# Kernel tuning notes

Measured on AMD Instinct MI355X. Metric: run time of the kernel, lower is better.

## Reference

```python
import jax, jax.numpy as jnp
import numpy as np

B, J, E = 4096, 32, 256

def setup_inputs() -> dict:
    key = jax.random.key(0)
    ks = jax.random.split(key, 7)
    return {
        "x": jax.random.normal(ks[0], (B, E), dtype=jnp.float32),
        "state": jax.random.normal(ks[1], (B, J * E), dtype=jnp.float32),
        "keys": jax.random.normal(ks[2], (J, E), dtype=jnp.float32) * 0.1,
        "U": jax.random.normal(ks[3], (E, E), dtype=jnp.float32) * 0.1,
        "V": jax.random.normal(ks[4], (E, E), dtype=jnp.float32) * 0.1,
        "W": jax.random.normal(ks[5], (E, E), dtype=jnp.float32) * 0.1,
        "bias": jax.random.normal(ks[6], (E,), dtype=jnp.float32) * 0.1,
    }

def reference(x, state, keys, U, V, W, bias):
    b, je = state.shape
    j = keys.shape[0]
    e = x.shape[1]
    s = state.reshape(b, j, e)                      # [B,J,E]
    # gate_j = sigmoid(<x, state_j> + <x, key_j>)
    gate = jax.nn.sigmoid(jnp.einsum('be,bje->bj', x, s)
                          + x @ keys.T)             # [B,J]
    # candidate_j = relu(U s_j + bias + W x + V k_j)
    cand = jax.nn.relu(jnp.einsum('bje,fe->bjf', s, U)
                       + bias
                       + (x @ W.T)[:, None, :]
                       + (keys @ V.T)[None, :, :])  # [B,J,E]
    s_next = s + gate[..., None] * cand
    norm = jnp.abs(jnp.linalg.norm(s_next, axis=-1, keepdims=True)) + 1e-8
    s_next = s_next / norm
    return s_next.reshape(b, je)
```

## Files before the change

kernel.cpp:

```cpp
#include <hip/hip_runtime.h>
#include <hip/hip_bf16.h>

typedef __bf16 bf16_t;
typedef __attribute__((ext_vector_type(8))) __bf16 bf16x8;
typedef __attribute__((ext_vector_type(4))) __bf16 bf16x4;
typedef __attribute__((ext_vector_type(4))) float f32x4;

#define E_DIM 256
#define J_DIM 32
#define B_DIM 4096
#define M_DIM (B_DIM * J_DIM)

#define XK_BLOCKS 512
#define CVT_BLOCKS 64
#define VKB_BLOCKS 32
#define PREP_GRID (XK_BLOCKS + 2 * CVT_BLOCKS + VKB_BLOCKS)

#define XK_LDA (E_DIM + 4)
#define LDB 40

__global__ __launch_bounds__(256) void prep_kernel(
    const float* __restrict__ x, const float* __restrict__ keys,
    const float* __restrict__ U, const float* __restrict__ V,
    const float* __restrict__ W, const float* __restrict__ bias,
    float* __restrict__ xk, float* __restrict__ vkb,
    bf16_t* __restrict__ Ubf, bf16_t* __restrict__ Wbf) {
    __shared__ float smem[(J_DIM + 8) * XK_LDA];
    int tid = threadIdx.x;
    int bid = blockIdx.x;
    if (bid < XK_BLOCKS) {
        float* sK = smem;
        float* sX = smem + J_DIM * XK_LDA;
        int b0 = bid * 8;
#pragma unroll
        for (int it = 0; it < 8; ++it) {
            int t = it * 256 + tid;
            int r = t >> 6, c = (t & 63) * 4;
            *(f32x4*)(sK + r * XK_LDA + c) = *(const f32x4*)(keys + (size_t)r * E_DIM + c);
        }
#pragma unroll
        for (int it = 0; it < 2; ++it) {
            int t = it * 256 + tid;
            int r = t >> 6, c = (t & 63) * 4;
            *(f32x4*)(sX + r * XK_LDA + c) =
                *(const f32x4*)(x + (size_t)(b0 + r) * E_DIM + c);
        }
        __syncthreads();
        int j = tid & 31, bl = tid >> 5;
        float acc = 0.f;
        for (int e = 0; e < E_DIM; e += 4) {
            f32x4 xv = *(const f32x4*)(sX + bl * XK_LDA + e);
            f32x4 kv = *(const f32x4*)(sK + j * XK_LDA + e);
#pragma unroll
            for (int i = 0; i < 4; ++i) acc += xv[i] * kv[i];
        }
        xk[(size_t)(b0 + bl) * J_DIM + j] = acc;
    } else if (bid < XK_BLOCKS + 2 * CVT_BLOCKS) {
        int cb = bid - XK_BLOCKS;
        const float* src = (cb < CVT_BLOCKS) ? U : W;
        bf16_t* dst = (cb < CVT_BLOCKS) ? Ubf : Wbf;
        int idx = (cb & (CVT_BLOCKS - 1)) * 1024 + tid * 4;
        f32x4 v = *(const f32x4*)(src + idx);
        bf16x4 o;
#pragma unroll
        for (int i = 0; i < 4; ++i) o[i] = (bf16_t)v[i];
        *(bf16x4*)(dst + idx) = o;
    } else {
        int j = bid - (XK_BLOCKS + 2 * CVT_BLOCKS);
        int f = tid;
        float* sk = smem;
        sk[f] = keys[(size_t)j * E_DIM + f];
        __syncthreads();
        float acc = bias[f];
        for (int e = 0; e < E_DIM; e += 4) {
            f32x4 vv = *(const f32x4*)(V + (size_t)f * E_DIM + e);
#pragma unroll
            for (int i = 0; i < 4; ++i) acc += vv[i] * sk[e + i];
        }
        vkb[(size_t)j * E_DIM + f] = acc;
    }
}

__global__ __launch_bounds__(256) void memcell_kernel(
    const float* __restrict__ x, const float* __restrict__ state,
    const bf16_t* __restrict__ Ubf, const bf16_t* __restrict__ Wbf,
    const float* __restrict__ xk, const float* __restrict__ vkb,
    float* __restrict__ out) {
    __shared__ __align__(16) bf16_t sB[2][E_DIM][LDB];
    int tid = threadIdx.x;
    int w = tid >> 6, lane = tid & 63, quad = lane >> 4, l15 = lane & 15;
    int m0 = blockIdx.x * 64;
    int bw = (m0 >> 5) + (w >> 1);
    f32x4 acc[16];
#pragma unroll
    for (int nt = 0; nt < 16; ++nt)
#pragma unroll
        for (int r = 0; r < 4; ++r) acc[nt][r] = 0.f;
    float gdot = 0.f;
    const float* sp = state + (size_t)(m0 + w * 16 + l15) * E_DIM + quad * 8;
    const float* xp = x + (size_t)bw * E_DIM + quad * 8;

    bf16x8 br0, br1, br2, br3;
    {
        const bf16_t* bp = Ubf + (size_t)tid * E_DIM;
        br0 = *(const bf16x8*)(bp);
        br1 = *(const bf16x8*)(bp + 8);
        br2 = *(const bf16x8*)(bp + 16);
        br3 = *(const bf16x8*)(bp + 24);
    }
    f32x4 a0 = *(const f32x4*)sp;
    f32x4 a1 = *(const f32x4*)(sp + 4);
    *(bf16x8*)(&sB[0][tid][0])  = br0;
    *(bf16x8*)(&sB[0][tid][8])  = br1;
    *(bf16x8*)(&sB[0][tid][16]) = br2;
    *(bf16x8*)(&sB[0][tid][24]) = br3;
    __syncthreads();

#pragma unroll
    for (int kc = 0; kc < 16; ++kc) {
        const int cur = kc & 1;
        if (kc < 15) {
            const int kn = kc + 1;
            const bf16_t* bp = (kn < 8 ? Ubf : Wbf) + (size_t)tid * E_DIM + (kn & 7) * 32;
            br0 = *(const bf16x8*)(bp);
            br1 = *(const bf16x8*)(bp + 8);
            br2 = *(const bf16x8*)(bp + 16);
            br3 = *(const bf16x8*)(bp + 24);
        }
        bf16x8 af;
        f32x4 n0, n1;
        if (kc < 8) {
            f32x4 xv0 = *(const f32x4*)(xp + kc * 32);
            f32x4 xv1 = *(const f32x4*)(xp + kc * 32 + 4);
            if (kc < 7) {
                n0 = *(const f32x4*)(sp + (kc + 1) * 32);
                n1 = *(const f32x4*)(sp + (kc + 1) * 32 + 4);
            }
#pragma unroll
            for (int i = 0; i < 4; ++i) { af[i] = (bf16_t)a0[i]; af[4 + i] = (bf16_t)a1[i]; }
#pragma unroll
            for (int i = 0; i < 4; ++i) gdot += a0[i] * xv0[i];
#pragma unroll
            for (int i = 0; i < 4; ++i) gdot += a1[i] * xv1[i];
        } else {
            const float* xq = xp + (kc - 8) * 32;
            f32x4 xa = *(const f32x4*)xq;
            f32x4 xb = *(const f32x4*)(xq + 4);
#pragma unroll
            for (int i = 0; i < 4; ++i) { af[i] = (bf16_t)xa[i]; af[4 + i] = (bf16_t)xb[i]; }
        }
#pragma unroll
        for (int nt = 0; nt < 16; ++nt) {
            bf16x8 bfr = *(const bf16x8*)(&sB[cur][nt * 16 + l15][quad * 8]);
            acc[nt] = __builtin_amdgcn_mfma_f32_16x16x32_bf16(af, bfr, acc[nt], 0, 0, 0);
        }
        if (kc < 8) { a0 = n0; a1 = n1; }
        if (kc < 15) {
            *(bf16x8*)(&sB[cur ^ 1][tid][0])  = br0;
            *(bf16x8*)(&sB[cur ^ 1][tid][8])  = br1;
            *(bf16x8*)(&sB[cur ^ 1][tid][16]) = br2;
            *(bf16x8*)(&sB[cur ^ 1][tid][24]) = br3;
            __syncthreads();
        }
    }

    gdot += __shfl_xor(gdot, 16);
    gdot += __shfl_xor(gdot, 32);
    float garg = gdot + xk[(size_t)bw * J_DIM + (w & 1) * 16 + l15];
    float gv = 1.f / (1.f + expf(-garg));
    float gate[4];
#pragma unroll
    for (int r = 0; r < 4; ++r) gate[r] = __shfl(gv, quad * 4 + r);
    float sumsq[4] = {0.f, 0.f, 0.f, 0.f};
#pragma unroll
    for (int nt = 0; nt < 16; ++nt) {
        int f = nt * 16 + l15;
#pragma unroll
        for (int r = 0; r < 4; ++r) {
            int rl = quad * 4 + r;
            int jidx = (w & 1) * 16 + rl;
            float c = acc[nt][r] + vkb[(size_t)jidx * E_DIM + f];
            c = fmaxf(c, 0.f);
            float sv = state[(size_t)(m0 + w * 16 + rl) * E_DIM + f];
            float t = fmaf(gate[r], c, sv);
            acc[nt][r] = t;
            sumsq[r] += t * t;
        }
    }
    float rn[4];
#pragma unroll
    for (int r = 0; r < 4; ++r) {
        float s2 = sumsq[r];
        s2 += __shfl_xor(s2, 1);
        s2 += __shfl_xor(s2, 2);
        s2 += __shfl_xor(s2, 4);
        s2 += __shfl_xor(s2, 8);
        rn[r] = 1.f / (sqrtf(s2) + 1e-8f);
    }
#pragma unroll
    for (int nt = 0; nt < 16; ++nt)
#pragma unroll
        for (int r = 0; r < 4; ++r)
            out[(size_t)(m0 + w * 16 + quad * 4 + r) * E_DIM + nt * 16 + l15] =
                acc[nt][r] * rn[r];
}

extern "C" void kernel_launch(void* const* d_in, const int* in_sizes, int n_in,
                              void* d_out, int out_size, void* d_ws, size_t ws_size,
                              hipStream_t stream) {
    const float* x     = (const float*)d_in[0];
    const float* state = (const float*)d_in[1];
    const float* keys  = (const float*)d_in[2];
    const float* U     = (const float*)d_in[3];
    const float* V     = (const float*)d_in[4];
    const float* W     = (const float*)d_in[5];
    const float* bias  = (const float*)d_in[6];
    float* out = (float*)d_out;

    float* wsf = (float*)d_ws;
    float* xk  = wsf;
    float* vkb = xk + (size_t)B_DIM * J_DIM;
    bf16_t* Ubf = (bf16_t*)(vkb + (size_t)J_DIM * E_DIM);
    bf16_t* Wbf = Ubf + (size_t)E_DIM * E_DIM;

    prep_kernel<<<PREP_GRID, 256, 0, stream>>>(x, keys, U, V, W, bias, xk, vkb, Ubf, Wbf);
    memcell_kernel<<<M_DIM / 64, 256, 0, stream>>>(x, state, Ubf, Wbf, xk, vkb, out);
}
```

Before: 364.0 us.

## Stage weights via global_load_lds and fold x·keys gate term into main kernel

Removes the separate x·keys precompute from the prep kernel and computes it inside the main kernel by adding keys to state in the gate dot product. The B-tile staging now uses direct global-to-LDS loads with an unpadded LDS layout, replacing the register round-trip and its register pressure. It also drops the state prefetch in favour of loads issued in the same iteration, and sets a launch bound of 4 blocks per SM. The unpadded LDS layout may cause bank conflicts on the fragment reads, and loading without prefetch may expose latency.

```diff
diff --git a/kernel.cpp b/kernel.cpp
--- a/kernel.cpp
+++ b/kernel.cpp
@@ -11,64 +11,24 @@
 #define B_DIM 4096
 #define M_DIM (B_DIM * J_DIM)
 
-#define XK_BLOCKS 512
-#define CVT_BLOCKS 64
-#define VKB_BLOCKS 32
-#define PREP_GRID (XK_BLOCKS + 2 * CVT_BLOCKS + VKB_BLOCKS)
-
-#define XK_LDA (E_DIM + 4)
-#define LDB 40
-
 __global__ __launch_bounds__(256) void prep_kernel(
-    const float* __restrict__ x, const float* __restrict__ keys,
-    const float* __restrict__ U, const float* __restrict__ V,
-    const float* __restrict__ W, const float* __restrict__ bias,
-    float* __restrict__ xk, float* __restrict__ vkb,
+    const float* __restrict__ keys, const float* __restrict__ U,
+    const float* __restrict__ V, const float* __restrict__ W,
+    const float* __restrict__ bias, float* __restrict__ vkb,
     bf16_t* __restrict__ Ubf, bf16_t* __restrict__ Wbf) {
-    __shared__ float smem[(J_DIM + 8) * XK_LDA];
-    int tid = threadIdx.x;
-    int bid = blockIdx.x;
-    if (bid < XK_BLOCKS) {
-        float* sK = smem;
-        float* sX = smem + J_DIM * XK_LDA;
-        int b0 = bid * 8;
-#pragma unroll
-        for (int it = 0; it < 8; ++it) {
-            int t = it * 256 + tid;
-            int r = t >> 6, c = (t & 63) * 4;
-            *(f32x4*)(sK + r * XK_LDA + c) = *(const f32x4*)(keys + (size_t)r * E_DIM + c);
-        }
-#pragma unroll
-        for (int it = 0; it < 2; ++it) {
-            int t = it * 256 + tid;
-            int r = t >> 6, c = (t & 63) * 4;
-            *(f32x4*)(sX + r * XK_LDA + c) =
-                *(const f32x4*)(x + (size_t)(b0 + r) * E_DIM + c);
-        }
-        __syncthreads();
-        int j = tid & 31, bl = tid >> 5;
-        float acc = 0.f;
-        for (int e = 0; e < E_DIM; e += 4) {
-            f32x4 xv = *(const f32x4*)(sX + bl * XK_LDA + e);
-            f32x4 kv = *(const f32x4*)(sK + j * XK_LDA + e);
-#pragma unroll
-            for (int i = 0; i < 4; ++i) acc += xv[i] * kv[i];
-        }
-        xk[(size_t)(b0 + bl) * J_DIM + j] = acc;
-    } else if (bid < XK_BLOCKS + 2 * CVT_BLOCKS) {
-        int cb = bid - XK_BLOCKS;
-        const float* src = (cb < CVT_BLOCKS) ? U : W;
-        bf16_t* dst = (cb < CVT_BLOCKS) ? Ubf : Wbf;
-        int idx = (cb & (CVT_BLOCKS - 1)) * 1024 + tid * 4;
+    int tid = threadIdx.x, bid = blockIdx.x;
+    if (bid < 128) {
+        const float* src = (bid < 64) ? U : W;
+        bf16_t* dst = (bid < 64) ? Ubf : Wbf;
+        int idx = (bid & 63) * 1024 + tid * 4;
         f32x4 v = *(const f32x4*)(src + idx);
         bf16x4 o;
 #pragma unroll
         for (int i = 0; i < 4; ++i) o[i] = (bf16_t)v[i];
         *(bf16x4*)(dst + idx) = o;
     } else {
-        int j = bid - (XK_BLOCKS + 2 * CVT_BLOCKS);
-        int f = tid;
-        float* sk = smem;
+        __shared__ float sk[E_DIM];
+        int j = bid - 128, f = tid;
         sk[f] = keys[(size_t)j * E_DIM + f];
         __syncthreads();
         float acc = bias[f];
@@ -81,16 +41,17 @@
     }
 }
 
-__global__ __launch_bounds__(256) void memcell_kernel(
+__global__ __launch_bounds__(256, 4) void memcell_kernel(
     const float* __restrict__ x, const float* __restrict__ state,
+    const float* __restrict__ keys,
     const bf16_t* __restrict__ Ubf, const bf16_t* __restrict__ Wbf,
-    const float* __restrict__ xk, const float* __restrict__ vkb,
-    float* __restrict__ out) {
-    __shared__ __align__(16) bf16_t sB[2][E_DIM][LDB];
+    const float* __restrict__ vkb, float* __restrict__ out) {
+    __shared__ __align__(16) bf16_t sB[2][E_DIM][32];
     int tid = threadIdx.x;
     int w = tid >> 6, lane = tid & 63, quad = lane >> 4, l15 = lane & 15;
     int m0 = blockIdx.x * 64;
     int bw = (m0 >> 5) + (w >> 1);
+    int jrow = (w & 1) * 16 + l15;
     f32x4 acc[16];
 #pragma unroll
     for (int nt = 0; nt < 16; ++nt)
@@ -99,53 +60,51 @@
     float gdot = 0.f;
     const float* sp = state + (size_t)(m0 + w * 16 + l15) * E_DIM + quad * 8;
     const float* xp = x + (size_t)bw * E_DIM + quad * 8;
+    const float* kp = keys + (size_t)jrow * E_DIM + quad * 8;
 
-    bf16x8 br0, br1, br2, br3;
-    {
-        const bf16_t* bp = Ubf + (size_t)tid * E_DIM;
-        br0 = *(const bf16x8*)(bp);
-        br1 = *(const bf16x8*)(bp + 8);
-        br2 = *(const bf16x8*)(bp + 16);
-        br3 = *(const bf16x8*)(bp + 24);
-    }
-    f32x4 a0 = *(const f32x4*)sp;
-    f32x4 a1 = *(const f32x4*)(sp + 4);
-    *(bf16x8*)(&sB[0][tid][0])  = br0;
-    *(bf16x8*)(&sB[0][tid][8])  = br1;
-    *(bf16x8*)(&sB[0][tid][16]) = br2;
-    *(bf16x8*)(&sB[0][tid][24]) = br3;
+    auto stage = [&](int buf, int kc) {
+        const bf16_t* src = (kc < 8) ? Ubf : Wbf;
+        const int koff = (kc & 7) * 32;
+        bf16_t* lb = &sB[buf][0][0];
+#pragma unroll
+        for (int it = 0; it < 4; ++it) {
+            int o = (it * 256 + tid) * 16;
+            int n = o >> 6;
+            int ce = (o & 63) >> 1;
+            const bf16_t* g = src + (size_t)n * E_DIM + koff + ce;
+            __builtin_amdgcn_global_load_lds(
+                (const __attribute__((address_space(1))) unsigned int*)g,
+                (__attribute__((address_space(3))) unsigned int*)(lb + (o >> 1)),
+                16, 0, 0);
+        }
+    };
+
+    stage(0, 0);
     __syncthreads();
 
 #pragma unroll
     for (int kc = 0; kc < 16; ++kc) {
         const int cur = kc & 1;
-        if (kc < 15) {
-            const int kn = kc + 1;
-            const bf16_t* bp = (kn < 8 ? Ubf : Wbf) + (size_t)tid * E_DIM + (kn & 7) * 32;
-            br0 = *(const bf16x8*)(bp);
-            br1 = *(const bf16x8*)(bp + 8);
-            br2 = *(const bf16x8*)(bp + 16);
-            br3 = *(const bf16x8*)(bp + 24);
-        }
+        if (kc < 15) stage(cur ^ 1, kc + 1);
         bf16x8 af;
-        f32x4 n0, n1;
         if (kc < 8) {
-            f32x4 xv0 = *(const f32x4*)(xp + kc * 32);
-            f32x4 xv1 = *(const f32x4*)(xp + kc * 32 + 4);
-            if (kc < 7) {
-                n0 = *(const f32x4*)(sp + (kc + 1) * 32);
-                n1 = *(const f32x4*)(sp + (kc + 1) * 32 + 4);
-            }
+            const int k0 = kc * 32;
+            f32x4 a0  = *(const f32x4*)(sp + k0);
+            f32x4 a1  = *(const f32x4*)(sp + k0 + 4);
+            f32x4 xv0 = *(const f32x4*)(xp + k0);
+            f32x4 xv1 = *(const f32x4*)(xp + k0 + 4);
+            f32x4 kv0 = *(const f32x4*)(kp + k0);
+            f32x4 kv1 = *(const f32x4*)(kp + k0 + 4);
 #pragma unroll
             for (int i = 0; i < 4; ++i) { af[i] = (bf16_t)a0[i]; af[4 + i] = (bf16_t)a1[i]; }
 #pragma unroll
-            for (int i = 0; i < 4; ++i) gdot += a0[i] * xv0[i];
+            for (int i = 0; i < 4; ++i) gdot += (a0[i] + kv0[i]) * xv0[i];
 #pragma unroll
-            for (int i = 0; i < 4; ++i) gdot += a1[i] * xv1[i];
+            for (int i = 0; i < 4; ++i) gdot += (a1[i] + kv1[i]) * xv1[i];
         } else {
-            const float* xq = xp + (kc - 8) * 32;
-            f32x4 xa = *(const f32x4*)xq;
-            f32x4 xb = *(const f32x4*)(xq + 4);
+            const int k0 = (kc - 8) * 32;
+            f32x4 xa = *(const f32x4*)(xp + k0);
+            f32x4 xb = *(const f32x4*)(xp + k0 + 4);
 #pragma unroll
             for (int i = 0; i < 4; ++i) { af[i] = (bf16_t)xa[i]; af[4 + i] = (bf16_t)xb[i]; }
         }
@@ -154,20 +113,12 @@
             bf16x8 bfr = *(const bf16x8*)(&sB[cur][nt * 16 + l15][quad * 8]);
             acc[nt] = __builtin_amdgcn_mfma_f32_16x16x32_bf16(af, bfr, acc[nt], 0, 0, 0);
         }
-        if (kc < 8) { a0 = n0; a1 = n1; }
-        if (kc < 15) {
-            *(bf16x8*)(&sB[cur ^ 1][tid][0])  = br0;
-            *(bf16x8*)(&sB[cur ^ 1][tid][8])  = br1;
-            *(bf16x8*)(&sB[cur ^ 1][tid][16]) = br2;
-            *(bf16x8*)(&sB[cur ^ 1][tid][24]) = br3;
-            __syncthreads();
-        }
+        __syncthreads();
     }
 
     gdot += __shfl_xor(gdot, 16);
     gdot += __shfl_xor(gdot, 32);
-    float garg = gdot + xk[(size_t)bw * J_DIM + (w & 1) * 16 + l15];
-    float gv = 1.f / (1.f + expf(-garg));
+    float gv = 1.f / (1.f + expf(-gdot));
     float gate[4];
 #pragma unroll
     for (int r = 0; r < 4; ++r) gate[r] = __shfl(gv, quad * 4 + r);
@@ -218,11 +169,10 @@
     float* out = (float*)d_out;
 
     float* wsf = (float*)d_ws;
-    float* xk  = wsf;
-    float* vkb = xk + (size_t)B_DIM * J_DIM;
+    float* vkb = wsf;
     bf16_t* Ubf = (bf16_t*)(vkb + (size_t)J_DIM * E_DIM);
     bf16_t* Wbf = Ubf + (size_t)E_DIM * E_DIM;
 
-    prep_kernel<<<PREP_GRID, 256, 0, stream>>>(x, keys, U, V, W, bias, xk, vkb, Ubf, Wbf);
-    memcell_kernel<<<M_DIM / 64, 256, 0, stream>>>(x, state, Ubf, Wbf, xk, vkb, out);
+    prep_kernel<<<160, 256, 0, stream>>>(keys, U, V, W, bias, vkb, Ubf, Wbf);
+    memcell_kernel<<<M_DIM / 64, 256, 0, stream>>>(x, state, keys, Ubf, Wbf, vkb, out);
 }
```

After: 558.8 us. +53.5%, slower.
